# Optimization experiments

Hardware: AMD Instinct MI355X
Metric: run time of the kernel (lower is better)

The kernel has to match this reference:

```python
import jax, jax.numpy as jnp
import numpy as np

N_NODES = 100000
N_EDGES = 1600000
NUM_GRAPHS = 64
IN_CH = 128
OUT_CH = 10


def setup_inputs() -> dict:
    key = jax.random.key(0)
    ks = jax.random.split(key, 12)
    s = 0.05
    x = jax.random.normal(ks[0], (N_NODES, IN_CH), dtype=jnp.float32)
    edge_index = jax.random.randint(ks[1], (2, N_EDGES), 0, N_NODES, dtype=jnp.int64)
    batch = jnp.sort(jax.random.randint(ks[2], (N_NODES,), 0, NUM_GRAPHS, dtype=jnp.int64))
    return {
        "x": x,
        "edge_index": edge_index,
        "batch": batch,
        "W1": jax.random.normal(ks[3], (IN_CH, 64), dtype=jnp.float32) * s,
        "b1": jnp.zeros((64,), dtype=jnp.float32),
        "W2": jax.random.normal(ks[4], (64, 64), dtype=jnp.float32) * s,
        "b2": jnp.zeros((64,), dtype=jnp.float32),
        "W3": jax.random.normal(ks[5], (64, 64), dtype=jnp.float32) * s,
        "b3": jnp.zeros((64,), dtype=jnp.float32),
        "W4": jax.random.normal(ks[6], (64, 128), dtype=jnp.float32) * s,
        "b4": jnp.zeros((128,), dtype=jnp.float32),
        "Wfc": jax.random.normal(ks[7], (128, OUT_CH), dtype=jnp.float32) * s,
        "bfc": jnp.zeros((OUT_CH,), dtype=jnp.float32),
    }


def _gin_agg(x, edge_index):
    # PyG GINConv (eps=0): h_i = x_i + sum_{j->i} x_j
    src, dst = edge_index[0], edge_index[1]
    agg = jax.ops.segment_sum(x[src], dst, num_segments=N_NODES)
    return x + agg


def reference(x, edge_index, batch, W1, b1, W2, b2, W3, b3, W4, b4, Wfc, bfc):
    # conv1: GINConv(Linear(in,64) -> ReLU -> Linear(64,64)), then outer ReLU
    h = _gin_agg(x, edge_index)
    h = jax.nn.relu(h @ W1 + b1) @ W2 + b2
    h = jax.nn.relu(h)
    # dropout is identity at eval time
    # conv2: GINConv(Linear(64,64) -> ReLU -> Linear(64,128))
    h = _gin_agg(h, edge_index)
    h = jax.nn.relu(h @ W3 + b3) @ W4 + b4
    # global mean pool over graphs
    sums = jax.ops.segment_sum(h, batch, num_segments=NUM_GRAPHS)
    counts = jax.ops.segment_sum(jnp.ones((N_NODES,), dtype=h.dtype), batch, num_segments=NUM_GRAPHS)
    pooled = sums / jnp.maximum(counts, 1.0)[:, None]
    logits = pooled @ Wfc + bfc
    return jax.nn.log_softmax(logits, axis=1)
```

## Files before the change

### kernel.cpp

```cpp
#include <hip/hip_runtime.h>
#include <cmath>

#define N_NODES    100000
#define N_EDGES    1600000
#define NUM_GRAPHS 64

#define BUCK_W     512
#define NBUCK      196
#define EPB        2048
#define NB1        782
#define GEMM_GS    782
#define AGG_NPB    64

typedef __attribute__((ext_vector_type(8))) short bf16x8;
typedef __attribute__((ext_vector_type(4))) float f32x4;
typedef __attribute__((ext_vector_type(2))) float f32x2;

__device__ __forceinline__ ushort f2bf(float x) {
    union { float f; uint u; } v; v.f = x;
    uint r = v.u + 0x7fffu + ((v.u >> 16) & 1u);
    return (ushort)(r >> 16);
}
__device__ __forceinline__ float bf2f(ushort u) {
    union { uint u; float f; } v; v.u = ((uint)u) << 16;
    return v.f;
}
__device__ __forceinline__ unsigned char f2fp8(float v) {
    int p = __builtin_amdgcn_cvt_pk_fp8_f32(v, v, 0, false);
    return (unsigned char)(p & 0xFF);
}
__device__ __forceinline__ void accum8_fp8(float* a, uint2 V) {
    f32x2 d0 = __builtin_amdgcn_cvt_pk_f32_fp8((int)V.x, false);
    f32x2 d1 = __builtin_amdgcn_cvt_pk_f32_fp8((int)V.x, true);
    f32x2 d2 = __builtin_amdgcn_cvt_pk_f32_fp8((int)V.y, false);
    f32x2 d3 = __builtin_amdgcn_cvt_pk_f32_fp8((int)V.y, true);
    a[0] += d0.x; a[1] += d0.y; a[2] += d1.x; a[3] += d1.y;
    a[4] += d2.x; a[5] += d2.y; a[6] += d3.x; a[7] += d3.y;
}

__global__ __launch_bounds__(256) void k1_hist_gemm(
    const int* __restrict__ dst, int* __restrict__ bcount,
    const float* __restrict__ x, const float* __restrict__ W1,
    unsigned char* __restrict__ y8)
{
    if (blockIdx.x < NB1) {
        __shared__ int shist[NBUCK];
        int tid = threadIdx.x;
        for (int i = tid; i < NBUCK; i += 256) shist[i] = 0;
        __syncthreads();
        int e0 = blockIdx.x * EPB + tid;
        #pragma unroll
        for (int k = 0; k < EPB / 256; ++k) {
            int e = e0 + k * 256;
            if (e < N_EDGES) atomicAdd(&shist[dst[e] >> 9], 1);
        }
        __syncthreads();
        for (int i = tid; i < NBUCK; i += 256)
            bcount[blockIdx.x * NBUCK + i] = shist[i];
        return;
    }
    int bid = blockIdx.x - NB1;
    int lane = threadIdx.x & 63, wave = threadIdx.x >> 6;
    int lg = lane >> 4, lm = lane & 15;

    bf16x8 Bf[4][4];
    #pragma unroll
    for (int kc = 0; kc < 4; ++kc)
        #pragma unroll
        for (int cb = 0; cb < 4; ++cb) {
            bf16x8 t;
            #pragma unroll
            for (int i = 0; i < 8; ++i)
                t[i] = (short)f2bf(W1[(kc * 32 + lg * 8 + i) * 64 + cb * 16 + lm]);
            Bf[kc][cb] = t;
        }

    const int ntiles = N_NODES / 16;
    for (int tile = bid * 4 + wave; tile < ntiles; tile += GEMM_GS * 4) {
        int r = tile * 16 + lm;
        f32x4 acc[4] = {};
        #pragma unroll
        for (int kc = 0; kc < 4; ++kc) {
            const float* p = x + (size_t)r * 128 + kc * 32 + lg * 8;
            float4 a0 = *(const float4*)p;
            float4 a1 = *(const float4*)(p + 4);
            bf16x8 af;
            af[0] = (short)f2bf(a0.x); af[1] = (short)f2bf(a0.y);
            af[2] = (short)f2bf(a0.z); af[3] = (short)f2bf(a0.w);
            af[4] = (short)f2bf(a1.x); af[5] = (short)f2bf(a1.y);
            af[6] = (short)f2bf(a1.z); af[7] = (short)f2bf(a1.w);
            #pragma unroll
            for (int cb = 0; cb < 4; ++cb)
                acc[cb] = __builtin_amdgcn_mfma_f32_16x16x32_bf16(af, Bf[kc][cb], acc[cb], 0, 0, 0);
        }
        #pragma unroll
        for (int cb = 0; cb < 4; ++cb)
            #pragma unroll
            for (int i = 0; i < 4; ++i)
                y8[(size_t)(tile * 16 + lg * 4 + i) * 64 + cb * 16 + lm] = f2fp8(acc[cb][i]);
    }
}

#define SCH 4
__global__ __launch_bounds__(256) void p2a_scan(
    const int* __restrict__ bcount, int* __restrict__ basetab,
    int* __restrict__ btot)
{
    __shared__ int sh[256];
    int b = blockIdx.x, tid = threadIdx.x;
    int v[SCH];
    int tsum = 0;
    #pragma unroll
    for (int j = 0; j < SCH; ++j) {
        int blk = tid * SCH + j;
        v[j] = (blk < NB1) ? bcount[(size_t)blk * NBUCK + b] : 0;
        tsum += v[j];
    }
    sh[tid] = tsum;
    __syncthreads();
    for (int off = 1; off < 256; off <<= 1) {
        int t = (tid >= off) ? sh[tid - off] : 0;
        __syncthreads();
        sh[tid] += t;
        __syncthreads();
    }
    if (tid == 255) btot[b] = sh[255];
    int excl = sh[tid] - tsum;
    #pragma unroll
    for (int j = 0; j < SCH; ++j) {
        int blk = tid * SCH + j;
        if (blk < NB1) basetab[(size_t)b * NB1 + blk] = excl;
        excl += v[j];
    }
}

__global__ __launch_bounds__(256) void p2b_scan(
    const int* __restrict__ btot, int* __restrict__ gbase,
    float* __restrict__ pooled)
{
    int tid = threadIdx.x;
    for (int i = tid; i < NUM_GRAPHS * 128; i += 256) pooled[i] = 0.0f;
    __shared__ int v[NBUCK];
    for (int j = tid; j < NBUCK; j += 256) v[j] = btot[j];
    __syncthreads();
    if (tid == 0) {
        int run = 0;
        for (int j = 0; j < NBUCK; ++j) { int t = v[j]; v[j] = run; run += t; }
        gbase[NBUCK] = run;
    }
    __syncthreads();
    for (int j = tid; j < NBUCK; j += 256) gbase[j] = v[j];
}

__global__ __launch_bounds__(256) void p3_partition(
    const int* __restrict__ src, const int* __restrict__ dst,
    const int* __restrict__ basetab, const int* __restrict__ gbase,
    uint* __restrict__ epack)
{
    __shared__ int cur[NBUCK];
    int blk = blockIdx.x, tid = threadIdx.x;
    for (int i = tid; i < NBUCK; i += 256)
        cur[i] = basetab[(size_t)i * NB1 + blk] + gbase[i];
    __syncthreads();
    int e0 = blk * EPB + tid;
    #pragma unroll
    for (int k = 0; k < EPB / 256; ++k) {
        int e = e0 + k * 256;
        if (e < N_EDGES) {
            int d = dst[e], s = src[e];
            int bin = d >> 9;
            int pos = atomicAdd(&cur[bin], 1);
            epack[pos] = ((uint)(d & 511) << 17) | (uint)s;
        }
    }
}

__global__ __launch_bounds__(256) void p4_fine(
    const uint* __restrict__ epack, const int* __restrict__ gbase,
    int* __restrict__ rowptr, int* __restrict__ esrc)
{
    __shared__ int hist[BUCK_W];
    int b = blockIdx.x, tid = threadIdx.x;
    int beg = gbase[b], end = gbase[b + 1];
    for (int i = tid; i < BUCK_W; i += 256) hist[i] = 0;
    __syncthreads();
    for (int e = beg + tid; e < end; e += 256)
        atomicAdd(&hist[epack[e] >> 17], 1);
    __syncthreads();
    if (tid == 0) {
        int run = 0;
        for (int i = 0; i < BUCK_W; ++i) { int t = hist[i]; hist[i] = run; run += t; }
    }
    __syncthreads();
    for (int i = tid; i < BUCK_W; i += 256) {
        int n = b * BUCK_W + i;
        if (n < N_NODES) rowptr[n] = beg + hist[i];
    }
    if (b == NBUCK - 1 && tid == 0) rowptr[N_NODES] = end;
    __syncthreads();
    for (int e = beg + tid; e < end; e += 256) {
        uint v = epack[e];
        int slot = beg + atomicAdd(&hist[v >> 17], 1);
        esrc[slot] = (int)(v & 0x1FFFFu);
    }
}

__global__ __launch_bounds__(256) void agg_fp8(
    const uint2* __restrict__ in8, uint4* __restrict__ out4,
    const int* __restrict__ rowptr, const int* __restrict__ esrc)
{
    __shared__ int pool;
    if (threadIdx.x == 0) pool = 0;
    __syncthreads();

    int sub = threadIdx.x & 7;
    int wl  = threadIdx.x & 63;
    int base = blockIdx.x * AGG_NPB;
    int nmax = min(AGG_NPB, N_NODES - base);

    for (;;) {
        int n = 0;
        if (sub == 0) n = atomicAdd(&pool, 1);
        n = __shfl(n, wl & 56, 64);
        if (n >= nmax) break;
        int node = base + n;

        float a[8] = {0, 0, 0, 0, 0, 0, 0, 0};
        accum8_fp8(a, in8[(size_t)node * 8 + sub]);

        int e = rowptr[node], end = rowptr[node + 1];
        for (; e + 8 <= end; e += 8) {
            int i0 = esrc[e],     i1 = esrc[e + 1], i2 = esrc[e + 2], i3 = esrc[e + 3];
            int i4 = esrc[e + 4], i5 = esrc[e + 5], i6 = esrc[e + 6], i7 = esrc[e + 7];
            uint2 v0 = in8[(size_t)i0 * 8 + sub];
            uint2 v1 = in8[(size_t)i1 * 8 + sub];
            uint2 v2 = in8[(size_t)i2 * 8 + sub];
            uint2 v3 = in8[(size_t)i3 * 8 + sub];
            uint2 v4 = in8[(size_t)i4 * 8 + sub];
            uint2 v5 = in8[(size_t)i5 * 8 + sub];
            uint2 v6 = in8[(size_t)i6 * 8 + sub];
            uint2 v7 = in8[(size_t)i7 * 8 + sub];
            accum8_fp8(a, v0); accum8_fp8(a, v1); accum8_fp8(a, v2); accum8_fp8(a, v3);
            accum8_fp8(a, v4); accum8_fp8(a, v5); accum8_fp8(a, v6); accum8_fp8(a, v7);
        }
        if (e + 4 <= end) {
            int i0 = esrc[e], i1 = esrc[e + 1], i2 = esrc[e + 2], i3 = esrc[e + 3];
            uint2 v0 = in8[(size_t)i0 * 8 + sub];
            uint2 v1 = in8[(size_t)i1 * 8 + sub];
            uint2 v2 = in8[(size_t)i2 * 8 + sub];
            uint2 v3 = in8[(size_t)i3 * 8 + sub];
            accum8_fp8(a, v0); accum8_fp8(a, v1); accum8_fp8(a, v2); accum8_fp8(a, v3);
            e += 4;
        }
        for (; e < end; ++e)
            accum8_fp8(a, in8[(size_t)esrc[e] * 8 + sub]);

        uint4 o;
        o.x = (uint)f2bf(a[0]) | ((uint)f2bf(a[1]) << 16);
        o.y = (uint)f2bf(a[2]) | ((uint)f2bf(a[3]) << 16);
        o.z = (uint)f2bf(a[4]) | ((uint)f2bf(a[5]) << 16);
        o.w = (uint)f2bf(a[6]) | ((uint)f2bf(a[7]) << 16);
        out4[(size_t)node * 8 + sub] = o;
    }
}

__global__ __launch_bounds__(256) void fused_mid(
    const ushort* __restrict__ yagg, const float* __restrict__ b1,
    const float* __restrict__ W2, const float* __restrict__ b2,
    const float* __restrict__ W3, unsigned char* __restrict__ z8)
{
    __shared__ __align__(16) float trs[4][16 * 68];
    int lane = threadIdx.x & 63, wave = threadIdx.x >> 6;
    int lg = lane >> 4, lm = lane & 15;

    bf16x8 B2[2][4], B3[2][4];
    #pragma unroll
    for (int kc = 0; kc < 2; ++kc)
        #pragma unroll
        for (int cb = 0; cb < 4; ++cb) {
            bf16x8 t2, t3;
            #pragma unroll
            for (int i = 0; i < 8; ++i) {
                int k = kc * 32 + lg * 8 + i;
                int cc = cb * 16 + lm;
                t2[i] = (short)f2bf(W2[k * 64 + cc]);
                t3[i] = (short)f2bf(W3[k * 64 + cc]);
            }
            B2[kc][cb] = t2; B3[kc][cb] = t3;
        }
    float b1r[2][8];
    #pragma unroll
    for (int kc = 0; kc < 2; ++kc)
        #pragma unroll
        for (int i = 0; i < 8; ++i)
            b1r[kc][i] = b1[kc * 32 + lg * 8 + i];
    float b2r[4];
    #pragma unroll
    for (int cb = 0; cb < 4; ++cb) b2r[cb] = b2[cb * 16 + lm];

    const int ntiles = N_NODES / 16;
    for (int tile = blockIdx.x * 4 + wave; tile < ntiles; tile += GEMM_GS * 4) {
        int r = tile * 16 + lm;
        bf16x8 A1[2];
        #pragma unroll
        for (int kc = 0; kc < 2; ++kc) {
            uint4 raw = *(const uint4*)(yagg + (size_t)r * 64 + kc * 32 + lg * 8);
            uint w[4] = {raw.x, raw.y, raw.z, raw.w};
            bf16x8 t;
            #pragma unroll
            for (int j = 0; j < 4; ++j) {
                float flo = bf2f((ushort)(w[j] & 0xffffu)) + b1r[kc][2 * j];
                float fhi = bf2f((ushort)(w[j] >> 16)) + b1r[kc][2 * j + 1];
                t[2 * j]     = (short)f2bf(fmaxf(flo, 0.0f));
                t[2 * j + 1] = (short)f2bf(fmaxf(fhi, 0.0f));
            }
            A1[kc] = t;
        }
        f32x4 acc[4] = {};
        #pragma unroll
        for (int kc = 0; kc < 2; ++kc)
            #pragma unroll
            for (int cb = 0; cb < 4; ++cb)
                acc[cb] = __builtin_amdgcn_mfma_f32_16x16x32_bf16(A1[kc], B2[kc][cb], acc[cb], 0, 0, 0);
        #pragma unroll
        for (int cb = 0; cb < 4; ++cb)
            #pragma unroll
            for (int i = 0; i < 4; ++i)
                trs[wave][(lg * 4 + i) * 68 + cb * 16 + lm] = fmaxf(acc[cb][i] + b2r[cb], 0.0f);
        bf16x8 A2[2];
        #pragma unroll
        for (int kc = 0; kc < 2; ++kc) {
            const float* p = &trs[wave][lm * 68 + kc * 32 + lg * 8];
            float4 u0 = *(const float4*)p;
            float4 u1 = *(const float4*)(p + 4);
            bf16x8 t;
            t[0] = (short)f2bf(u0.x); t[1] = (short)f2bf(u0.y);
            t[2] = (short)f2bf(u0.z); t[3] = (short)f2bf(u0.w);
            t[4] = (short)f2bf(u1.x); t[5] = (short)f2bf(u1.y);
            t[6] = (short)f2bf(u1.z); t[7] = (short)f2bf(u1.w);
            A2[kc] = t;
        }
        f32x4 acc2[4] = {};
        #pragma unroll
        for (int kc = 0; kc < 2; ++kc)
            #pragma unroll
            for (int cb = 0; cb < 4; ++cb)
                acc2[cb] = __builtin_amdgcn_mfma_f32_16x16x32_bf16(A2[kc], B3[kc][cb], acc2[cb], 0, 0, 0);
        #pragma unroll
        for (int cb = 0; cb < 4; ++cb)
            #pragma unroll
            for (int i = 0; i < 4; ++i)
                z8[(size_t)(tile * 16 + lg * 4 + i) * 64 + cb * 16 + lm] = f2fp8(acc2[cb][i]);
    }
}

__global__ __launch_bounds__(256) void k4_mfma_pool(
    const ushort* __restrict__ zagg, const float* __restrict__ b3,
    const float* __restrict__ W4, const float* __restrict__ b4,
    const int* __restrict__ batch, float* __restrict__ pooled)
{
    int lane = threadIdx.x & 63, wave = threadIdx.x >> 6;
    int lg = lane >> 4, lm = lane & 15;

    bf16x8 B4[2][8];
    #pragma unroll
    for (int kc = 0; kc < 2; ++kc)
        #pragma unroll
        for (int cb = 0; cb < 8; ++cb) {
            bf16x8 t;
            #pragma unroll
            for (int i = 0; i < 8; ++i)
                t[i] = (short)f2bf(W4[(kc * 32 + lg * 8 + i) * 128 + cb * 16 + lm]);
            B4[kc][cb] = t;
        }
    float b3r[2][8];
    #pragma unroll
    for (int kc = 0; kc < 2; ++kc)
        #pragma unroll
        for (int i = 0; i < 8; ++i)
            b3r[kc][i] = b3[kc * 32 + lg * 8 + i];
    float b4r[8];
    #pragma unroll
    for (int cb = 0; cb < 8; ++cb) b4r[cb] = b4[cb * 16 + lm];

    const int NT = N_NODES / 16;
    const int TPW = 4;
    int w = blockIdx.x * 4 + wave;
    int t0 = w * TPW;
    if (t0 >= NT) return;
    int t1 = min(t0 + TPW, NT);

    float pacc[8] = {0, 0, 0, 0, 0, 0, 0, 0};
    int curg = batch[t0 * 16];

#define FLUSH(G) do {                                                     \
        _Pragma("unroll")                                                 \
        for (int cb = 0; cb < 8; ++cb) {                                  \
            float v = pacc[cb];                                           \
            v += __shfl_xor(v, 16, 64);                                   \
            v += __shfl_xor(v, 32, 64);                                   \
            if (lane < 16) unsafeAtomicAdd(&pooled[(G) * 128 + cb * 16 + lm], v); \
            pacc[cb] = 0.0f;                                              \
        }                                                                 \
    } while (0)

    for (int t = t0; t < t1; ++t) {
        int rbase = t * 16;
        int r = rbase + lm;
        bf16x8 A[2];
        #pragma unroll
        for (int kc = 0; kc < 2; ++kc) {
            uint4 raw = *(const uint4*)(zagg + (size_t)r * 64 + kc * 32 + lg * 8);
            uint wv[4] = {raw.x, raw.y, raw.z, raw.w};
            bf16x8 tt;
            #pragma unroll
            for (int j = 0; j < 4; ++j) {
                float flo = bf2f((ushort)(wv[j] & 0xffffu)) + b3r[kc][2 * j];
                float fhi = bf2f((ushort)(wv[j] >> 16))    + b3r[kc][2 * j + 1];
                tt[2 * j]     = (short)f2bf(fmaxf(flo, 0.0f));
                tt[2 * j + 1] = (short)f2bf(fmaxf(fhi, 0.0f));
            }
            A[kc] = tt;
        }
        f32x4 acc[8] = {};
        #pragma unroll
        for (int kc = 0; kc < 2; ++kc)
            #pragma unroll
            for (int cb = 0; cb < 8; ++cb)
                acc[cb] = __builtin_amdgcn_mfma_f32_16x16x32_bf16(A[kc], B4[kc][cb], acc[cb], 0, 0, 0);

        int g0 = batch[rbase], g15 = batch[rbase + 15];
        if (g0 != curg) { FLUSH(curg); curg = g0; }
        if (g0 == g15) {
            #pragma unroll
            for (int cb = 0; cb < 8; ++cb)
                pacc[cb] += acc[cb][0] + acc[cb][1] + acc[cb][2] + acc[cb][3]
                            + 4.0f * b4r[cb];
        } else {
            FLUSH(curg);
            #pragma unroll
            for (int i = 0; i < 4; ++i) {
                int gi = batch[rbase + lg * 4 + i];
                #pragma unroll
                for (int cb = 0; cb < 8; ++cb)
                    unsafeAtomicAdd(&pooled[gi * 128 + cb * 16 + lm],
                                    acc[cb][i] + b4r[cb]);
            }
            curg = g15;
        }
    }
    FLUSH(curg);
#undef FLUSH
}

__global__ void head_kernel(
    const float* __restrict__ pooled, const int* __restrict__ batch,
    const float* __restrict__ Wfc, const float* __restrict__ bfc,
    float* __restrict__ out)
{
    int g = threadIdx.x;
    if (g >= NUM_GRAPHS) return;

    int lo = 0, hi = N_NODES;
    while (lo < hi) { int mid = (lo + hi) >> 1; if (batch[mid] < g) lo = mid + 1; else hi = mid; }
    int beg = lo;
    lo = 0; hi = N_NODES;
    while (lo < hi) { int mid = (lo + hi) >> 1; if (batch[mid] < g + 1) lo = mid + 1; else hi = mid; }
    int cnt = lo - beg;
    float inv = 1.0f / fmaxf((float)cnt, 1.0f);

    float logits[10];
    for (int o = 0; o < 10; ++o) {
        float acc = 0.0f;
        for (int k = 0; k < 128; ++k)
            acc = fmaf(pooled[g * 128 + k], Wfc[k * 10 + o], acc);
        logits[o] = acc * inv + bfc[o];
    }
    float m = -INFINITY;
    for (int o = 0; o < 10; ++o) m = fmaxf(m, logits[o]);
    float s = 0.0f;
    for (int o = 0; o < 10; ++o) s += expf(logits[o] - m);
    float ls = logf(s);
    for (int o = 0; o < 10; ++o) out[g * 10 + o] = logits[o] - m - ls;
}

extern "C" void kernel_launch(void* const* d_in, const int* in_sizes, int n_in,
                              void* d_out, int out_size, void* d_ws, size_t ws_size,
                              hipStream_t stream)
{
    const float* x     = (const float*)d_in[0];
    const int*   ei    = (const int*)d_in[1];
    const int*   src   = ei;
    const int*   dst   = ei + N_EDGES;
    const int*   batch = (const int*)d_in[2];
    const float* W1  = (const float*)d_in[3];
    const float* b1  = (const float*)d_in[4];
    const float* W2  = (const float*)d_in[5];
    const float* b2  = (const float*)d_in[6];
    const float* W3  = (const float*)d_in[7];
    const float* b3  = (const float*)d_in[8];
    const float* W4  = (const float*)d_in[9];
    const float* b4  = (const float*)d_in[10];
    const float* Wfc = (const float*)d_in[11];
    const float* bfc = (const float*)d_in[12];
    float* out = (float*)d_out;

    char* ws = (char*)d_ws;
    unsigned char* yfp8 = (unsigned char*)(ws);
    unsigned char* zfp8 = (unsigned char*)(ws + 6400000);
    ushort* yagg  = (ushort*)(ws + 12800000);
    ushort* zagg  = (ushort*)(ws + 25600000);
    int*  esrc    = (int*) (ws + 38400000);
    uint* epack   = (uint*)(ws + 44800000);
    int*  rowptr  = (int*) (ws + 51200000);
    int*  bcount  = (int*) (ws + 51600016);
    int*  basetab = (int*) (ws + 52213104);
    int*  btot    = (int*) (ws + 52826192);
    int*  gbase   = (int*) (ws + 52826976);
    float* pooled = (float*)(ws + 52827776);

    k1_hist_gemm<<<NB1 + GEMM_GS, 256, 0, stream>>>(dst, bcount, x, W1, yfp8);
    p2a_scan<<<NBUCK, 256, 0, stream>>>(bcount, basetab, btot);
    p2b_scan<<<1, 256, 0, stream>>>(btot, gbase, pooled);
    p3_partition<<<NB1, 256, 0, stream>>>(src, dst, basetab, gbase, epack);
    p4_fine<<<NBUCK, 256, 0, stream>>>(epack, gbase, rowptr, esrc);

    agg_fp8<<<(N_NODES + AGG_NPB - 1) / AGG_NPB, 256, 0, stream>>>(
        (const uint2*)yfp8, (uint4*)yagg, rowptr, esrc);
    fused_mid<<<GEMM_GS, 256, 0, stream>>>(yagg, b1, W2, b2, W3, zfp8);

    agg_fp8<<<(N_NODES + AGG_NPB - 1) / AGG_NPB, 256, 0, stream>>>(
        (const uint2*)zfp8, (uint4*)zagg, rowptr, esrc);
    {
        const int NT = N_NODES / 16;
        const int TPW = 4;
        int blocks = (NT + 4 * TPW - 1) / (4 * TPW);
        k4_mfma_pool<<<blocks, 256, 0, stream>>>(zagg, b3, W4, b4, batch, pooled);
    }

    head_kernel<<<1, 64, 0, stream>>>(pooled, batch, Wfc, bfc, out);
}
```

Before: 173.6 us.

## Fuse bias+ReLU into aggregation storing fp8, and stage partition writes in LDS

```diff
diff --git a/kernel.cpp b/kernel.cpp
--- a/kernel.cpp
+++ b/kernel.cpp
@@ -28,6 +28,13 @@
 __device__ __forceinline__ unsigned char f2fp8(float v) {
     int p = __builtin_amdgcn_cvt_pk_fp8_f32(v, v, 0, false);
     return (unsigned char)(p & 0xFF);
+}
+__device__ __forceinline__ uint2 pack8_fp8(const float* r) {
+    uint lo = (uint)__builtin_amdgcn_cvt_pk_fp8_f32(r[0], r[1], 0, false);
+    lo = (uint)__builtin_amdgcn_cvt_pk_fp8_f32(r[2], r[3], (int)lo, true);
+    uint hi = (uint)__builtin_amdgcn_cvt_pk_fp8_f32(r[4], r[5], 0, false);
+    hi = (uint)__builtin_amdgcn_cvt_pk_fp8_f32(r[6], r[7], (int)hi, true);
+    uint2 o; o.x = lo; o.y = hi; return o;
 }
 __device__ __forceinline__ void accum8_fp8(float* a, uint2 V) {
     f32x2 d0 = __builtin_amdgcn_cvt_pk_f32_fp8((int)V.x, false);
@@ -36,6 +43,18 @@
     f32x2 d3 = __builtin_amdgcn_cvt_pk_f32_fp8((int)V.y, true);
     a[0] += d0.x; a[1] += d0.y; a[2] += d1.x; a[3] += d1.y;
     a[4] += d2.x; a[5] += d2.y; a[6] += d3.x; a[7] += d3.y;
+}
+__device__ __forceinline__ bf16x8 fp8_to_bf16x8(uint2 V) {
+    f32x2 d0 = __builtin_amdgcn_cvt_pk_f32_fp8((int)V.x, false);
+    f32x2 d1 = __builtin_amdgcn_cvt_pk_f32_fp8((int)V.x, true);
+    f32x2 d2 = __builtin_amdgcn_cvt_pk_f32_fp8((int)V.y, false);
+    f32x2 d3 = __builtin_amdgcn_cvt_pk_f32_fp8((int)V.y, true);
+    bf16x8 t;
+    t[0] = (short)f2bf(d0.x); t[1] = (short)f2bf(d0.y);
+    t[2] = (short)f2bf(d1.x); t[3] = (short)f2bf(d1.y);
+    t[4] = (short)f2bf(d2.x); t[5] = (short)f2bf(d2.y);
+    t[6] = (short)f2bf(d3.x); t[7] = (short)f2bf(d3.y);
+    return t;
 }
 
 __global__ __launch_bounds__(256) void k1_hist_gemm(
@@ -157,21 +176,53 @@
     const int* __restrict__ basetab, const int* __restrict__ gbase,
     uint* __restrict__ epack)
 {
-    __shared__ int cur[NBUCK];
+    __shared__ int shist[NBUCK];
+    __shared__ int scur[NBUCK];
+    __shared__ int sbase[NBUCK];
+    __shared__ uint lbuf[EPB];
+    __shared__ unsigned char lbin[EPB];
+
     int blk = blockIdx.x, tid = threadIdx.x;
-    for (int i = tid; i < NBUCK; i += 256)
-        cur[i] = basetab[(size_t)i * NB1 + blk] + gbase[i];
-    __syncthreads();
-    int e0 = blk * EPB + tid;
+    int cnt = min(EPB, N_EDGES - blk * EPB);
+
+    for (int i = tid; i < NBUCK; i += 256) shist[i] = 0;
+    __syncthreads();
+
+    uint mypack[EPB / 256];
+    int  mybin[EPB / 256];
     #pragma unroll
     for (int k = 0; k < EPB / 256; ++k) {
-        int e = e0 + k * 256;
+        int e = blk * EPB + tid + k * 256;
         if (e < N_EDGES) {
             int d = dst[e], s = src[e];
-            int bin = d >> 9;
-            int pos = atomicAdd(&cur[bin], 1);
-            epack[pos] = ((uint)(d & 511) << 17) | (uint)s;
-        }
+            mybin[k] = d >> 9;
+            mypack[k] = ((uint)(d & 511) << 17) | (uint)s;
+            atomicAdd(&shist[mybin[k]], 1);
+        } else mybin[k] = -1;
+    }
+    __syncthreads();
+    if (tid == 0) {
+        int run = 0;
+        for (int i = 0; i < NBUCK; ++i) { int t = shist[i]; shist[i] = run; run += t; }
+    }
+    __syncthreads();
+    for (int i = tid; i < NBUCK; i += 256) {
+        scur[i] = shist[i];
+        sbase[i] = basetab[(size_t)i * NB1 + blk] + gbase[i] - shist[i];
+    }
+    __syncthreads();
+    #pragma unroll
+    for (int k = 0; k < EPB / 256; ++k) {
+        if (mybin[k] >= 0) {
+            int p = atomicAdd(&scur[mybin[k]], 1);
+            lbuf[p] = mypack[k];
+            lbin[p] = (unsigned char)mybin[k];
+        }
+    }
+    __syncthreads();
+    for (int j = tid; j < cnt; j += 256) {
+        int bin = lbin[j];
+        epack[sbase[bin] + j] = lbuf[j];
     }
 }
 
@@ -206,7 +257,8 @@
 }
 
 __global__ __launch_bounds__(256) void agg_fp8(
-    const uint2* __restrict__ in8, uint4* __restrict__ out4,
+    const uint2* __restrict__ in8, uint2* __restrict__ outact,
+    const float* __restrict__ bias,
     const int* __restrict__ rowptr, const int* __restrict__ esrc)
 {
     __shared__ int pool;
@@ -215,6 +267,10 @@
 
     int sub = threadIdx.x & 7;
     int wl  = threadIdx.x & 63;
+    float bg[8];
+    #pragma unroll
+    for (int j = 0; j < 8; ++j) bg[j] = bias[sub * 8 + j];
+
     int base = blockIdx.x * AGG_NPB;
     int nmax = min(AGG_NPB, N_NODES - base);
 
@@ -255,19 +311,17 @@
         for (; e < end; ++e)
             accum8_fp8(a, in8[(size_t)esrc[e] * 8 + sub]);
 
-        uint4 o;
-        o.x = (uint)f2bf(a[0]) | ((uint)f2bf(a[1]) << 16);
-        o.y = (uint)f2bf(a[2]) | ((uint)f2bf(a[3]) << 16);
-        o.z = (uint)f2bf(a[4]) | ((uint)f2bf(a[5]) << 16);
-        o.w = (uint)f2bf(a[6]) | ((uint)f2bf(a[7]) << 16);
-        out4[(size_t)node * 8 + sub] = o;
+        float r[8];
+        #pragma unroll
+        for (int j = 0; j < 8; ++j) r[j] = fmaxf(a[j] + bg[j], 0.0f);
+        outact[(size_t)node * 8 + sub] = pack8_fp8(r);
     }
 }
 
 __global__ __launch_bounds__(256) void fused_mid(
-    const ushort* __restrict__ yagg, const float* __restrict__ b1,
-    const float* __restrict__ W2, const float* __restrict__ b2,
-    const float* __restrict__ W3, unsigned char* __restrict__ z8)
+    const uint2* __restrict__ yact, const float* __restrict__ W2,
+    const float* __restrict__ b2, const float* __restrict__ W3,
+    unsigned char* __restrict__ z8)
 {
     __shared__ __align__(16) float trs[4][16 * 68];
     int lane = threadIdx.x & 63, wave = threadIdx.x >> 6;
@@ -288,12 +342,6 @@
             }
             B2[kc][cb] = t2; B3[kc][cb] = t3;
         }
-    float b1r[2][8];
-    #pragma unroll
-    for (int kc = 0; kc < 2; ++kc)
-        #pragma unroll
-        for (int i = 0; i < 8; ++i)
-            b1r[kc][i] = b1[kc * 32 + lg * 8 + i];
     float b2r[4];
     #pragma unroll
     for (int cb = 0; cb < 4; ++cb) b2r[cb] = b2[cb * 16 + lm];
@@ -303,19 +351,8 @@
         int r = tile * 16 + lm;
         bf16x8 A1[2];
         #pragma unroll
-        for (int kc = 0; kc < 2; ++kc) {
-            uint4 raw = *(const uint4*)(yagg + (size_t)r * 64 + kc * 32 + lg * 8);
-            uint w[4] = {raw.x, raw.y, raw.z, raw.w};
-            bf16x8 t;
-            #pragma unroll
-            for (int j = 0; j < 4; ++j) {
-                float flo = bf2f((ushort)(w[j] & 0xffffu)) + b1r[kc][2 * j];
-                float fhi = bf2f((ushort)(w[j] >> 16)) + b1r[kc][2 * j + 1];
-                t[2 * j]     = (short)f2bf(fmaxf(flo, 0.0f));
-                t[2 * j + 1] = (short)f2bf(fmaxf(fhi, 0.0f));
-            }
-            A1[kc] = t;
-        }
+        for (int kc = 0; kc < 2; ++kc)
+            A1[kc] = fp8_to_bf16x8(yact[(size_t)r * 8 + kc * 4 + lg]);
         f32x4 acc[4] = {};
         #pragma unroll
         for (int kc = 0; kc < 2; ++kc)
@@ -355,9 +392,9 @@
 }
 
 __global__ __launch_bounds__(256) void k4_mfma_pool(
-    const ushort* __restrict__ zagg, const float* __restrict__ b3,
-    const float* __restrict__ W4, const float* __restrict__ b4,
-    const int* __restrict__ batch, float* __restrict__ pooled)
+    const uint2* __restrict__ zact, const float* __restrict__ W4,
+    const float* __restrict__ b4, const int* __restrict__ batch,
+    float* __restrict__ pooled)
 {
     int lane = threadIdx.x & 63, wave = threadIdx.x >> 6;
     int lg = lane >> 4, lm = lane & 15;
@@ -373,12 +410,6 @@
                 t[i] = (short)f2bf(W4[(kc * 32 + lg * 8 + i) * 128 + cb * 16 + lm]);
             B4[kc][cb] = t;
         }
-    float b3r[2][8];
-    #pragma unroll
-    for (int kc = 0; kc < 2; ++kc)
-        #pragma unroll
-        for (int i = 0; i < 8; ++i)
-            b3r[kc][i] = b3[kc * 32 + lg * 8 + i];
     float b4r[8];
     #pragma unroll
     for (int cb = 0; cb < 8; ++cb) b4r[cb] = b4[cb * 16 + lm];
@@ -409,19 +440,8 @@
         int r = rbase + lm;
         bf16x8 A[2];
         #pragma unroll
-        for (int kc = 0; kc < 2; ++kc) {
-            uint4 raw = *(const uint4*)(zagg + (size_t)r * 64 + kc * 32 + lg * 8);
-            uint wv[4] = {raw.x, raw.y, raw.z, raw.w};
-            bf16x8 tt;
-            #pragma unroll
-            for (int j = 0; j < 4; ++j) {
-                float flo = bf2f((ushort)(wv[j] & 0xffffu)) + b3r[kc][2 * j];
-                float fhi = bf2f((ushort)(wv[j] >> 16))    + b3r[kc][2 * j + 1];
-                tt[2 * j]     = (short)f2bf(fmaxf(flo, 0.0f));
-                tt[2 * j + 1] = (short)f2bf(fmaxf(fhi, 0.0f));
-            }
-            A[kc] = tt;
-        }
+        for (int kc = 0; kc < 2; ++kc)
+            A[kc] = fp8_to_bf16x8(zact[(size_t)r * 8 + kc * 4 + lg]);
         f32x4 acc[8] = {};
         #pragma unroll
         for (int kc = 0; kc < 2; ++kc)
@@ -508,16 +528,16 @@
     char* ws = (char*)d_ws;
     unsigned char* yfp8 = (unsigned char*)(ws);
     unsigned char* zfp8 = (unsigned char*)(ws + 6400000);
-    ushort* yagg  = (ushort*)(ws + 12800000);
-    ushort* zagg  = (ushort*)(ws + 25600000);
-    int*  esrc    = (int*) (ws + 38400000);
-    uint* epack   = (uint*)(ws + 44800000);
-    int*  rowptr  = (int*) (ws + 51200000);
-    int*  bcount  = (int*) (ws + 51600016);
-    int*  basetab = (int*) (ws + 52213104);
-    int*  btot    = (int*) (ws + 52826192);
-    int*  gbase   = (int*) (ws + 52826976);
-    float* pooled = (float*)(ws + 52827776);
+    uint2* yact  = (uint2*)(ws + 12800000);
+    uint2* zact  = (uint2*)(ws + 19200000);
+    int*  esrc    = (int*) (ws + 25600000);
+    uint* epack   = (uint*)(ws + 32000000);
+    int*  rowptr  = (int*) (ws + 38400000);
+    int*  bcount  = (int*) (ws + 38800016);
+    int*  basetab = (int*) (ws + 39413104);
+    int*  btot    = (int*) (ws + 40026192);
+    int*  gbase   = (int*) (ws + 40026976);
+    float* pooled = (float*)(ws + 40027776);
 
     k1_hist_gemm<<<NB1 + GEMM_GS, 256, 0, stream>>>(dst, bcount, x, W1, yfp8);
     p2a_scan<<<NBUCK, 256, 0, stream>>>(bcount, basetab, btot);
@@ -526,16 +546,16 @@
     p4_fine<<<NBUCK, 256, 0, stream>>>(epack, gbase, rowptr, esrc);
 
     agg_fp8<<<(N_NODES + AGG_NPB - 1) / AGG_NPB, 256, 0, stream>>>(
-        (const uint2*)yfp8, (uint4*)yagg, rowptr, esrc);
-    fused_mid<<<GEMM_GS, 256, 0, stream>>>(yagg, b1, W2, b2, W3, zfp8);
+        (const uint2*)yfp8, yact, b1, rowptr, esrc);
+    fused_mid<<<GEMM_GS, 256, 0, stream>>>(yact, W2, b2, W3, zfp8);
 
     agg_fp8<<<(N_NODES + AGG_NPB - 1) / AGG_NPB, 256, 0, stream>>>(
-        (const uint2*)zfp8, (uint4*)zagg, rowptr, esrc);
+        (const uint2*)zfp8, zact, b3, rowptr, esrc);
     {
         const int NT = N_NODES / 16;
         const int TPW = 4;
         int blocks = (NT + 4 * TPW - 1) / (4 * TPW);
-        k4_mfma_pool<<<blocks, 256, 0, stream>>>(zagg, b3, W4, b4, batch, pooled);
+        k4_mfma_pool<<<blocks, 256, 0, stream>>>(zact, W4, b4, batch, pooled);
     }
 
     head_kernel<<<1, 64, 0, stream>>>(pooled, batch, Wfc, bfc, out);
```

New measurement: 179.3 us. +3.2%, slower.
